# Optimization experiments

Hardware: AMD Instinct MI355X
Metric: run time of the kernel (lower is better)

## Reference

```python
import jax, jax.numpy as jnp
from jax import lax
import numpy as np

N, C, H, W = 8, 32, 64, 64
KS, NB = 7, 6            # kernel_size, num_bases
TB = (KS // 2) * NB      # total_bases = 18
BC = TB * NB             # bc_dim = 108
INTER = max(64, BC // 2) # 64
OUT = 64
PAD = KS // 2
EPS = 1e-5


def conv3x3(x, w, b):
    # x: (N,Cin,H,W), w: (Cout,Cin,3,3)
    y = lax.conv_general_dilated(x, w, (1, 1), [(1, 1), (1, 1)],
                                 dimension_numbers=('NCHW', 'OIHW', 'NCHW'))
    return y + b[None, :, None, None]


def batchnorm(x, g, b):
    # training-mode BN: batch stats over (N,H,W)
    mu = jnp.mean(x, axis=(0, 2, 3), keepdims=True)
    var = jnp.var(x, axis=(0, 2, 3), keepdims=True)
    return (x - mu) * lax.rsqrt(var + EPS) * g[None, :, None, None] + b[None, :, None, None]


def setup_inputs() -> dict:
    key = jax.random.key(0)
    ks = jax.random.split(key, 12)
    s = 0.05
    # random bases as in get_random_bases: (TB, KS*KS), zero-mean-ish rows
    f = jax.random.normal(ks[0], (TB, KS * KS), dtype=jnp.float32)
    bases = f - jnp.mean(f, axis=1, keepdims=True) / jnp.std(f, axis=1, keepdims=True)
    return {
        'x': jax.random.normal(ks[1], (N, C, H, W), dtype=jnp.float32),
        'conv1_w': jax.random.normal(ks[2], (INTER, C, 3, 3), dtype=jnp.float32) * s,
        'conv1_b': jax.random.normal(ks[3], (INTER,), dtype=jnp.float32) * s,
        'bn1_g': jnp.ones((INTER,), jnp.float32),
        'bn1_b': jnp.zeros((INTER,), jnp.float32),
        'conv2_w': jax.random.normal(ks[4], (BC, INTER, 3, 3), dtype=jnp.float32) * s,
        'conv2_b': jax.random.normal(ks[5], (BC,), dtype=jnp.float32) * s,
        'bn2_g': jnp.ones((BC,), jnp.float32),
        'bn2_b': jnp.zeros((BC,), jnp.float32),
        'bases': bases,
        'out_w': jax.random.normal(ks[6], (OUT, C * NB), dtype=jnp.float32) * s,
        'out_b': jax.random.normal(ks[7], (OUT,), dtype=jnp.float32) * s,
    }


def reference(x, conv1_w, conv1_b, bn1_g, bn1_b, conv2_w, conv2_b,
              bn2_g, bn2_b, bases, out_w, out_b):
    # bases_net: conv3x3 -> BN -> tanh -> conv3x3 -> BN -> tanh
    h = jnp.tanh(batchnorm(conv3x3(x, conv1_w, conv1_b), bn1_g, bn1_b))
    coef = jnp.tanh(batchnorm(conv3x3(h, conv2_w, conv2_b), bn2_g, bn2_b))
    # (N, BC, H, W) -> (N, NB, TB, H, W) -> (N, H, W, NB, TB)
    coef = coef.reshape(N, NB, TB, H, W).transpose(0, 3, 4, 1, 2)
    # atoms: (coef[...,None] * bases).sum(-2).transpose(-1,-2) => (N,H,W,KS^2,NB)
    atoms = jnp.einsum('nhwmt,tk->nhwkm', coef, bases)
    # unfold: channel-major (C, ks, ks) flattened, matching F.unfold
    patches = lax.conv_general_dilated_patches(
        x, (KS, KS), (1, 1), [(PAD, PAD), (PAD, PAD)],
        dimension_numbers=('NCHW', 'OIHW', 'NCHW'))  # (N, C*KS*KS, H, W)
    patches = patches.reshape(N, C, KS * KS, H, W)
    # per-pixel contraction over ks^2: (N,H,W,C,NB)
    bases_out = jnp.einsum('nckhw,nhwkm->nhwcm', patches, atoms)
    bases_out = bases_out.reshape(N, H, W, C * NB)
    out = jnp.einsum('nhwd,od->nohw', bases_out, out_w) + out_b[None, :, None, None]
    return out
```

## Files before the change

### kernel.cpp

```cpp
#include <hip/hip_runtime.h>
#include <hip/hip_bf16.h>

#define N_ 8
#define C_ 32
#define H_ 64
#define W_ 64
#define HW_ (H_*W_)
#define NHW_ (N_*HW_)
#define INTER_ 64
#define BC_ 108
#define KS_ 7
#define K2_ (KS_*KS_)
#define NB_ 6
#define TB_ 18
#define OUT_ 64
#define DDIM_ (C_*NB_)
#define P2CH_ 288

typedef __attribute__((ext_vector_type(8))) short short8;
typedef __attribute__((ext_vector_type(4))) float f32x4;

__device__ __forceinline__ unsigned short f2bf(float f) {
    union { float f; unsigned u; } v; v.f = f;
    unsigned r = v.u + 0x7fffu + ((v.u >> 16) & 1u);
    return (unsigned short)(r >> 16);
}
__device__ __forceinline__ float bf2f(unsigned short h) {
    return __uint_as_float((unsigned int)h << 16);
}

__device__ __forceinline__ short8 frag4(const unsigned int* p) {
    union { unsigned int u[4]; short8 s; } v;
    v.u[0] = p[0]; v.u[1] = p[1]; v.u[2] = p[2]; v.u[3] = p[3];
    return v.s;
}

__inline__ __device__ float wave_reduce_sum(float v) {
    #pragma unroll
    for (int off = 32; off > 0; off >>= 1) v += __shfl_down(v, off);
    return v;
}

__global__ __launch_bounds__(256) void k_front(const float* __restrict__ x,
                                               const float* __restrict__ bases,
                                               const float* __restrict__ w1,
                                               const float* __restrict__ w2,
                                               const float* __restrict__ ow,
                                               unsigned short* __restrict__ xb,
                                               unsigned short* __restrict__ wb1,
                                               unsigned short* __restrict__ wb2,
                                               unsigned short* __restrict__ wbp,
                                               unsigned int* __restrict__ P2) {
    __shared__ __align__(16) char smem[70 * 44 * 4];
    int bid = blockIdx.x, t = threadIdx.x;

    if (bid < 1024) {
        float (*sx)[44] = (float(*)[44])smem;
        int rq = bid & 3;
        int c  = (bid >> 2) & 31;
        int n  = bid >> 7;
        int lane = t & 63, wv = t >> 6;
        int r0 = rq << 4;

        const float* xc = x + (((size_t)n * C_ + c) << 12);
        #pragma unroll
        for (int j = 0; j < 6; j++) {
            int p = wv + 4 * j;
            if (p < 22) {
                int grow = r0 - 3 + p;
                bool rowok = (grow >= 0 && grow < H_);
                int wx = lane - 3;
                float v = 0.f;
                if (rowok && wx >= 0) v = xc[(grow << 6) + wx];
                sx[lane][p] = v;
                if (lane < 6) {
                    int wx2 = 61 + lane;
                    float v2 = 0.f;
                    if (rowok && wx2 < W_) v2 = xc[(grow << 6) + wx2];
                    sx[64 + lane][p] = v2;
                }
            }
        }
        __syncthreads();

        int rb = wv * 4;
        float a0[9][4], a1[9][4];
        #pragma unroll
        for (int tp = 0; tp < 9; tp++)
            #pragma unroll
            for (int rr = 0; rr < 4; rr++) { a0[tp][rr] = 0.f; a1[tp][rr] = 0.f; }

        #pragma unroll 1
        for (int kx = 0; kx < 7; kx++) {
            float rw[12];
            const float* sp = &sx[lane + kx][rb];
            #pragma unroll
            for (int qq = 0; qq < 3; qq++) {
                float4 r4 = *(const float4*)(sp + qq * 4);
                rw[qq * 4 + 0] = r4.x; rw[qq * 4 + 1] = r4.y;
                rw[qq * 4 + 2] = r4.z; rw[qq * 4 + 3] = r4.w;
            }
            #pragma unroll
            for (int tp = 0; tp < 9; tp++) {
                #pragma unroll
                for (int ky = 0; ky < 7; ky++) {
                    float w0 = bases[(2 * tp) * K2_ + ky * 7 + kx];
                    float w1v = bases[(2 * tp + 1) * K2_ + ky * 7 + kx];
                    #pragma unroll
                    for (int rr = 0; rr < 4; rr++) {
                        float xv = rw[rr + ky];
                        a0[tp][rr] += xv * w0;
                        a1[tp][rr] += xv * w1v;
                    }
                }
            }
        }

        #pragma unroll
        for (int tp = 0; tp < 9; tp++)
            #pragma unroll
            for (int rr = 0; rr < 4; rr++) {
                int gr = r0 + rb + rr;
                unsigned int pk = (unsigned int)f2bf(a0[tp][rr]) | ((unsigned int)f2bf(a1[tp][rr]) << 16);
                P2[(((size_t)n * P2CH_ + tp * 32 + c) << 12) + (gr << 6) + lane] = pk;
            }
    } else {
        int pbid = bid - 1024;
        if (pbid < 512) {
            unsigned short* sT = (unsigned short*)smem;
            int n = pbid >> 6, hw0 = (pbid << 6) & 4095;
            for (int i = t; i < 2048; i += 256) {
                int c = i >> 6, px = i & 63;
                float v = x[(((size_t)n * C_ + c) << 12) + hw0 + px];
                sT[px * 36 + c] = f2bf(v);
            }
            __syncthreads();
            unsigned int* xd = (unsigned int*)xb;
            for (int i = t; i < 1024; i += 256) {
                int px = i >> 4, cw = i & 15;
                unsigned int lo = sT[px * 36 + cw * 2], hi = sT[px * 36 + cw * 2 + 1];
                xd[(((size_t)n << 12) + hw0 + px) * 16 + cw] = lo | (hi << 16);
            }
        } else if (pbid < 584) {
            int i = (pbid - 512) * 256 + t;
            int ci = i & 31, co = (i >> 5) & 63, s = i >> 11;
            wb1[i] = f2bf(w1[((co << 5) + ci) * 9 + s]);
        } else if (pbid < 872) {
            int i = (pbid - 584) * 256 + t;
            int ci = i & 63, co = (i >> 6) & 127, s = i >> 13;
            unsigned short v = 0;
            if (co < BC_) v = f2bf(w2[((co << 6) + ci) * 9 + s]);
            wb2[i] = v;
        } else {
            int i = (pbid - 872) * 256 + t;
            if (i < OUT_ * DDIM_) {
                float v = ow[i];
                unsigned short hi = f2bf(v);
                wbp[i] = hi;
                wbp[OUT_ * DDIM_ + i] = f2bf(v - bf2f(hi));
            }
        }
    }
}

template<int CIN, int COG, int ROWS, int WPAD, int NCOQ>
__global__ __launch_bounds__(256) void k_conv3(const unsigned short* __restrict__ xb,
                                               const unsigned short* __restrict__ wb,
                                               const float* __restrict__ bias,
                                               float* __restrict__ y,
                                               int COUT_real) {
    constexpr int CPAD = CIN + 8;
    constexpr int NSLC = (ROWS + 2) * 66;
    constexpr int MT = COG / 16;
    constexpr int NTW = ROWS;
    constexpr int KSTEPS = CIN / 32;
    __shared__ unsigned short sx[NSLC * CPAD];
    __shared__ unsigned short sw[9 * COG * CPAD];

    int bid = blockIdx.x;
    int coq = bid % NCOQ;
    int rp = (bid / NCOQ) % (H_ / ROWS);
    int n = bid / (NCOQ * (H_ / ROWS));
    int h0 = rp * ROWS;
    int co0 = coq * COG;
    int t = threadIdx.x;
    int lane = t & 63, wv = t >> 6;
    int q = lane >> 4, n15 = lane & 15;

    {
        const unsigned int* xg = (const unsigned int*)xb + (size_t)n * HW_ * (CIN / 2);
        unsigned int* sxd = (unsigned int*)sx;
        constexpr int DW = CIN / 2;
        constexpr int DWPT = DW / 8;
        int part = t & 7;
        for (int sl = (t >> 3); sl < NSLC; sl += 32) {
            int r = sl / 66, col = sl % 66;
            int hh = h0 - 1 + r, ww = col - 1;
            unsigned int v[DWPT];
            #pragma unroll
            for (int i = 0; i < DWPT; i++) v[i] = 0;
            if (hh >= 0 && hh < H_ && ww >= 0 && ww < W_) {
                const unsigned int* gp = xg + (size_t)(hh * W_ + ww) * DW + part * DWPT;
                #pragma unroll
                for (int i = 0; i < DWPT; i++) v[i] = gp[i];
            }
            unsigned int* d = sxd + sl * (CPAD / 2) + part * DWPT;
            #pragma unroll
            for (int i = 0; i < DWPT; i++) d[i] = v[i];
        }
    }
    {
        const unsigned int* wg = (const unsigned int*)wb;
        unsigned int* swd = (unsigned int*)sw;
        constexpr int TOT = 9 * COG * (CIN / 2);
        for (int e = t; e < TOT; e += 256) {
            int s_co = e / (CIN / 2), cw = e % (CIN / 2);
            int s = s_co / COG, co = s_co % COG;
            swd[s_co * (CPAD / 2) + cw] = wg[((size_t)s * WPAD + co0 + co) * (CIN / 2) + cw];
        }
    }
    __syncthreads();

    f32x4 acc[NTW][MT];
    #pragma unroll
    for (int a = 0; a < NTW; a++)
        #pragma unroll
        for (int m = 0; m < MT; m++) acc[a][m] = (f32x4){0.f, 0.f, 0.f, 0.f};

    #pragma unroll
    for (int s = 0; s < 9; s++) {
        int dy = s / 3, dx = s % 3;
        #pragma unroll
        for (int kc = 0; kc < KSTEPS; kc++) {
            int ci0 = kc * 32;
            short8 bfr[NTW];
            #pragma unroll
            for (int ntl = 0; ntl < NTW; ntl++) {
                int nt = wv * NTW + ntl;
                int r_out = nt >> 2, col0 = (nt & 3) * 16;
                bfr[ntl] = *(const short8*)(sx + ((r_out + dy) * 66 + col0 + n15 + dx) * CPAD + ci0 + q * 8);
            }
            #pragma unroll
            for (int mt = 0; mt < MT; mt++) {
                short8 afr = *(const short8*)(sw + ((s * COG) + mt * 16 + n15) * CPAD + ci0 + q * 8);
                #pragma unroll
                for (int ntl = 0; ntl < NTW; ntl++)
                    acc[ntl][mt] = __builtin_amdgcn_mfma_f32_16x16x32_bf16(afr, bfr[ntl], acc[ntl][mt], 0, 0, 0);
            }
        }
    }

    #pragma unroll
    for (int ntl = 0; ntl < NTW; ntl++) {
        int nt = wv * NTW + ntl;
        int h = h0 + (nt >> 2), wcol = (nt & 3) * 16 + n15;
        #pragma unroll
        for (int mt = 0; mt < MT; mt++) {
            #pragma unroll
            for (int reg = 0; reg < 4; reg++) {
                int co = co0 + mt * 16 + q * 4 + reg;
                if (co < COUT_real)
                    y[(((size_t)n * COUT_real + co) << 12) + h * W_ + wcol] = acc[ntl][mt][reg] + bias[co];
            }
        }
    }
}

__global__ __launch_bounds__(256) void k_bnpart(const float* __restrict__ y,
                                                float2* __restrict__ part, int Cout) {
    int bid = blockIdx.x;
    int c = bid >> 3, n = bid & 7;
    int t = threadIdx.x;
    const float* p = y + (((size_t)n * Cout + c) << 12) + t * 16;
    float s = 0.f, s2 = 0.f;
    #pragma unroll
    for (int j = 0; j < 4; j++) {
        float4 v = *(const float4*)(p + j * 4);
        s += v.x + v.y + v.z + v.w;
        s2 += v.x * v.x + v.y * v.y + v.z * v.z + v.w * v.w;
    }
    s = wave_reduce_sum(s);
    s2 = wave_reduce_sum(s2);
    __shared__ float sm[8];
    int wid = t >> 6, lane = t & 63;
    if (lane == 0) { sm[wid] = s; sm[4 + wid] = s2; }
    __syncthreads();
    if (t == 0) {
        float2 r;
        r.x = sm[0] + sm[1] + sm[2] + sm[3];
        r.y = sm[4] + sm[5] + sm[6] + sm[7];
        part[c * 8 + n] = r;
    }
}

__global__ __launch_bounds__(256) void k_bntr(const float* __restrict__ y1,
                                              const float2* __restrict__ part,
                                              const float* __restrict__ g,
                                              const float* __restrict__ bb,
                                              unsigned short* __restrict__ y1b) {
    __shared__ unsigned short sT[64 * 68];
    __shared__ float scs[INTER_], shs[INTER_];
    int bid = blockIdx.x, t = threadIdx.x;
    int n = bid >> 6, hw0 = (bid << 6) & 4095;
    if (t < INTER_) {
        float s = 0.f, s2 = 0.f;
        #pragma unroll
        for (int j = 0; j < 8; j++) { float2 p = part[t * 8 + j]; s += p.x; s2 += p.y; }
        float mu = s / (float)NHW_, var = s2 / (float)NHW_ - mu * mu;
        float sc = g[t] * rsqrtf(var + 1e-5f);
        scs[t] = sc; shs[t] = bb[t] - mu * sc;
    }
    __syncthreads();
    for (int i = t; i < 4096; i += 256) {
        int c = i >> 6, px = i & 63;
        float v = y1[(((size_t)n * INTER_ + c) << 12) + hw0 + px];
        sT[px * 68 + c] = f2bf(tanhf(v * scs[c] + shs[c]));
    }
    __syncthreads();
    unsigned int* yd = (unsigned int*)y1b;
    for (int i = t; i < 2048; i += 256) {
        int px = i >> 5, cw = i & 31;
        unsigned int lo = sT[px * 68 + cw * 2], hi = sT[px * 68 + cw * 2 + 1];
        yd[(((size_t)n << 12) + hw0 + px) * 32 + cw] = lo | (hi << 16);
    }
}

#define YPAD_ 97
__global__ __launch_bounds__(256) void k_ytail(const float* __restrict__ y2,
                                               const float2* __restrict__ part,
                                               const float* __restrict__ g,
                                               const float* __restrict__ bb,
                                               const unsigned int* __restrict__ P2,
                                               const unsigned short* __restrict__ wbp,
                                               const float* __restrict__ out_b,
                                               float* __restrict__ out) {
    __shared__ float scs[BC_], shs[BC_];
    __shared__ float cfs[BC_][32];
    __shared__ unsigned int sYh[32 * YPAD_];
    __shared__ unsigned int sYl[32 * YPAD_];

    int bid = blockIdx.x;
    int n = bid >> 7, px0 = (bid & 127) << 5;
    int t = threadIdx.x;

    int px = t & 31, cg = t >> 5;
    unsigned int u[4][9];
    {
        const unsigned int* Pb = P2 + (((size_t)n * P2CH_) << 12) + px0 + px;
        #pragma unroll
        for (int cc = 0; cc < 4; cc++) {
            int c = cg * 4 + cc;
            #pragma unroll
            for (int tp = 0; tp < 9; tp++)
                u[cc][tp] = Pb[(size_t)(tp * 32 + c) << 12];
        }
    }

    if (t < BC_) {
        float s = 0.f, s2 = 0.f;
        #pragma unroll
        for (int j = 0; j < 8; j++) { float2 p = part[t * 8 + j]; s += p.x; s2 += p.y; }
        float mu = s / (float)NHW_, var = s2 / (float)NHW_ - mu * mu;
        float sc = g[t] * rsqrtf(var + 1e-5f);
        scs[t] = sc; shs[t] = bb[t] - mu * sc;
    }
    __syncthreads();

    for (int i = t; i < BC_ * 32; i += 256) {
        int ch = i >> 5, pxx = i & 31;
        float v = y2[(((size_t)n * BC_ + ch) << 12) + px0 + pxx];
        cfs[ch][pxx] = tanhf(v * scs[ch] + shs[ch]);
    }
    __syncthreads();

    {
        float pv[4][TB_];
        #pragma unroll
        for (int cc = 0; cc < 4; cc++)
            #pragma unroll
            for (int tp = 0; tp < 9; tp++) {
                pv[cc][2 * tp]     = __uint_as_float(u[cc][tp] << 16);
                pv[cc][2 * tp + 1] = __uint_as_float(u[cc][tp] & 0xffff0000u);
            }
        float ym[4][NB_];
        #pragma unroll
        for (int cc = 0; cc < 4; cc++)
            #pragma unroll
            for (int m = 0; m < NB_; m++) ym[cc][m] = 0.f;
        #pragma unroll
        for (int m = 0; m < NB_; m++)
            #pragma unroll
            for (int tt = 0; tt < TB_; tt++) {
                float cfv = cfs[m * TB_ + tt][px];
                #pragma unroll
                for (int cc = 0; cc < 4; cc++)
                    ym[cc][m] += cfv * pv[cc][tt];
            }
        #pragma unroll
        for (int cc = 0; cc < 4; cc++) {
            int c = cg * 4 + cc;
            #pragma unroll
            for (int j = 0; j < 3; j++) {
                unsigned short h0 = f2bf(ym[cc][2 * j]);
                unsigned short h1 = f2bf(ym[cc][2 * j + 1]);
                unsigned short l0 = f2bf(ym[cc][2 * j] - bf2f(h0));
                unsigned short l1 = f2bf(ym[cc][2 * j + 1] - bf2f(h1));
                sYh[px * YPAD_ + c * 3 + j] = (unsigned int)h0 | ((unsigned int)h1 << 16);
                sYl[px * YPAD_ + c * 3 + j] = (unsigned int)l0 | ((unsigned int)l1 << 16);
            }
        }
    }
    __syncthreads();

    int lane = t & 63, wv = t >> 6;
    int q = lane >> 4, n15 = lane & 15;
    f32x4 acc[2];
    acc[0] = (f32x4){0.f, 0.f, 0.f, 0.f};
    acc[1] = (f32x4){0.f, 0.f, 0.f, 0.f};
    #pragma unroll
    for (int ks = 0; ks < 6; ks++) {
        short8 ah = *(const short8*)(wbp + (wv * 16 + n15) * DDIM_ + ks * 32 + q * 8);
        short8 al = *(const short8*)(wbp + OUT_ * DDIM_ + (wv * 16 + n15) * DDIM_ + ks * 32 + q * 8);
        #pragma unroll
        for (int nt = 0; nt < 2; nt++) {
            short8 bh = frag4(sYh + (nt * 16 + n15) * YPAD_ + ks * 16 + q * 4);
            short8 bl = frag4(sYl + (nt * 16 + n15) * YPAD_ + ks * 16 + q * 4);
            acc[nt] = __builtin_amdgcn_mfma_f32_16x16x32_bf16(ah, bh, acc[nt], 0, 0, 0);
            acc[nt] = __builtin_amdgcn_mfma_f32_16x16x32_bf16(ah, bl, acc[nt], 0, 0, 0);
            acc[nt] = __builtin_amdgcn_mfma_f32_16x16x32_bf16(al, bh, acc[nt], 0, 0, 0);
        }
    }
    #pragma unroll
    for (int nt = 0; nt < 2; nt++)
        #pragma unroll
        for (int reg = 0; reg < 4; reg++) {
            int o = wv * 16 + q * 4 + reg;
            out[(((size_t)n * OUT_ + o) << 12) + px0 + nt * 16 + n15] = acc[nt][reg] + out_b[o];
        }
}

extern "C" void kernel_launch(void* const* d_in, const int* in_sizes, int n_in,
                              void* d_out, int out_size, void* d_ws, size_t ws_size,
                              hipStream_t stream) {
    const float* x       = (const float*)d_in[0];
    const float* conv1_w = (const float*)d_in[1];
    const float* conv1_b = (const float*)d_in[2];
    const float* bn1_g   = (const float*)d_in[3];
    const float* bn1_b   = (const float*)d_in[4];
    const float* conv2_w = (const float*)d_in[5];
    const float* conv2_b = (const float*)d_in[6];
    const float* bn2_g   = (const float*)d_in[7];
    const float* bn2_b   = (const float*)d_in[8];
    const float* bases   = (const float*)d_in[9];
    const float* out_w   = (const float*)d_in[10];
    const float* out_b   = (const float*)d_in[11];
    float* out = (float*)d_out;

    float* y1  = (float*)d_ws;
    float* y2  = y1 + (size_t)N_ * INTER_ * HW_;
    unsigned int* P2 = (unsigned int*)(y2 + (size_t)N_ * BC_ * HW_);
    unsigned short* xb  = (unsigned short*)(P2 + (size_t)N_ * P2CH_ * HW_);
    unsigned short* y1b = xb + (size_t)NHW_ * C_;
    unsigned short* wb1 = y1b + (size_t)NHW_ * INTER_;
    unsigned short* wb2 = wb1 + 9 * 64 * 32;
    unsigned short* wbp = wb2 + 9 * 128 * 64;
    float2* part1 = (float2*)(wbp + 2 * OUT_ * DDIM_);
    float2* part2 = part1 + INTER_ * 8;

    k_front<<<1944, 256, 0, stream>>>(x, bases, conv1_w, conv2_w, out_w,
                                      xb, wb1, wb2, wbp, P2);

    k_conv3<C_, 64, 1, 64, 1><<<N_ * 64, 256, 0, stream>>>(
        xb, wb1, conv1_b, y1, INTER_);
    k_bnpart<<<INTER_ * 8, 256, 0, stream>>>(y1, part1, INTER_);
    k_bntr<<<512, 256, 0, stream>>>(y1, part1, bn1_g, bn1_b, y1b);

    k_conv3<INTER_, 16, 2, 128, 7><<<N_ * 32 * 7, 256, 0, stream>>>(
        y1b, wb2, conv2_b, y2, BC_);
    k_bnpart<<<BC_ * 8, 256, 0, stream>>>(y2, part2, BC_);

    k_ytail<<<1024, 256, 0, stream>>>(y2, (const float2*)part2, bn2_g, bn2_b,
                                      P2, wbp, out_b, out);
}
```

Before: 196.2 us.

## Co-schedule patch-basis precompute with conv2 in one merged launch

The front kernel is split: the weight and input conversion stays in a small k_prep launch, while the per-channel patch×bases precompute (P2) moves into a new k_cpv kernel that interleaves it with conv2 blocks (7 conv blocks and 4 precompute blocks per group of 11). The aim is to overlap the ALU-heavy P2 work with the MFMA conv2 work and take it off the critical path ahead of conv1. In exchange, the shared-memory footprint is sized for the larger branch (about 58KB), which may lower occupancy for the conv blocks and makes the two workloads compete for the same compute units.

```diff
diff --git a/kernel.cpp b/kernel.cpp
--- a/kernel.cpp
+++ b/kernel.cpp
@@ -41,25 +41,249 @@
     return v;
 }
 
-__global__ __launch_bounds__(256) void k_front(const float* __restrict__ x,
-                                               const float* __restrict__ bases,
-                                               const float* __restrict__ w1,
-                                               const float* __restrict__ w2,
-                                               const float* __restrict__ ow,
-                                               unsigned short* __restrict__ xb,
-                                               unsigned short* __restrict__ wb1,
-                                               unsigned short* __restrict__ wb2,
-                                               unsigned short* __restrict__ wbp,
-                                               unsigned int* __restrict__ P2) {
-    __shared__ __align__(16) char smem[70 * 44 * 4];
+__global__ __launch_bounds__(256) void k_prep(const float* __restrict__ x,
+                                              const float* __restrict__ w1,
+                                              const float* __restrict__ w2,
+                                              const float* __restrict__ ow,
+                                              unsigned short* __restrict__ xb,
+                                              unsigned short* __restrict__ wb1,
+                                              unsigned short* __restrict__ wb2,
+                                              unsigned short* __restrict__ wbp) {
+    __shared__ unsigned short sT[64 * 36];
+    int pbid = blockIdx.x, t = threadIdx.x;
+    if (pbid < 512) {
+        int n = pbid >> 6, hw0 = (pbid << 6) & 4095;
+        for (int i = t; i < 2048; i += 256) {
+            int c = i >> 6, px = i & 63;
+            float v = x[(((size_t)n * C_ + c) << 12) + hw0 + px];
+            sT[px * 36 + c] = f2bf(v);
+        }
+        __syncthreads();
+        unsigned int* xd = (unsigned int*)xb;
+        for (int i = t; i < 1024; i += 256) {
+            int px = i >> 4, cw = i & 15;
+            unsigned int lo = sT[px * 36 + cw * 2], hi = sT[px * 36 + cw * 2 + 1];
+            xd[(((size_t)n << 12) + hw0 + px) * 16 + cw] = lo | (hi << 16);
+        }
+    } else if (pbid < 584) {
+        int i = (pbid - 512) * 256 + t;
+        int ci = i & 31, co = (i >> 5) & 63, s = i >> 11;
+        wb1[i] = f2bf(w1[((co << 5) + ci) * 9 + s]);
+    } else if (pbid < 872) {
+        int i = (pbid - 584) * 256 + t;
+        int ci = i & 63, co = (i >> 6) & 127, s = i >> 13;
+        unsigned short v = 0;
+        if (co < BC_) v = f2bf(w2[((co << 6) + ci) * 9 + s]);
+        wb2[i] = v;
+    } else {
+        int i = (pbid - 872) * 256 + t;
+        if (i < OUT_ * DDIM_) {
+            float v = ow[i];
+            unsigned short hi = f2bf(v);
+            wbp[i] = hi;
+            wbp[OUT_ * DDIM_ + i] = f2bf(v - bf2f(hi));
+        }
+    }
+}
+
+template<int CIN, int COG, int ROWS, int WPAD, int NCOQ>
+__global__ __launch_bounds__(256) void k_conv3(const unsigned short* __restrict__ xb,
+                                               const unsigned short* __restrict__ wb,
+                                               const float* __restrict__ bias,
+                                               float* __restrict__ y,
+                                               int COUT_real) {
+    constexpr int CPAD = CIN + 8;
+    constexpr int NSLC = (ROWS + 2) * 66;
+    constexpr int MT = COG / 16;
+    constexpr int NTW = ROWS;
+    constexpr int KSTEPS = CIN / 32;
+    __shared__ unsigned short sx[NSLC * CPAD];
+    __shared__ unsigned short sw[9 * COG * CPAD];
+
+    int bid = blockIdx.x;
+    int coq = bid % NCOQ;
+    int rp = (bid / NCOQ) % (H_ / ROWS);
+    int n = bid / (NCOQ * (H_ / ROWS));
+    int h0 = rp * ROWS;
+    int co0 = coq * COG;
+    int t = threadIdx.x;
+    int lane = t & 63, wv = t >> 6;
+    int q = lane >> 4, n15 = lane & 15;
+
+    {
+        const unsigned int* xg = (const unsigned int*)xb + (size_t)n * HW_ * (CIN / 2);
+        unsigned int* sxd = (unsigned int*)sx;
+        constexpr int DW = CIN / 2;
+        constexpr int DWPT = DW / 8;
+        int part = t & 7;
+        for (int sl = (t >> 3); sl < NSLC; sl += 32) {
+            int r = sl / 66, col = sl % 66;
+            int hh = h0 - 1 + r, ww = col - 1;
+            unsigned int v[DWPT];
+            #pragma unroll
+            for (int i = 0; i < DWPT; i++) v[i] = 0;
+            if (hh >= 0 && hh < H_ && ww >= 0 && ww < W_) {
+                const unsigned int* gp = xg + (size_t)(hh * W_ + ww) * DW + part * DWPT;
+                #pragma unroll
+                for (int i = 0; i < DWPT; i++) v[i] = gp[i];
+            }
+            unsigned int* d = sxd + sl * (CPAD / 2) + part * DWPT;
+            #pragma unroll
+            for (int i = 0; i < DWPT; i++) d[i] = v[i];
+        }
+    }
+    {
+        const unsigned int* wg = (const unsigned int*)wb;
+        unsigned int* swd = (unsigned int*)sw;
+        constexpr int TOT = 9 * COG * (CIN / 2);
+        for (int e = t; e < TOT; e += 256) {
+            int s_co = e / (CIN / 2), cw = e % (CIN / 2);
+            int s = s_co / COG, co = s_co % COG;
+            swd[s_co * (CPAD / 2) + cw] = wg[((size_t)s * WPAD + co0 + co) * (CIN / 2) + cw];
+        }
+    }
+    __syncthreads();
+
+    f32x4 acc[NTW][MT];
+    #pragma unroll
+    for (int a = 0; a < NTW; a++)
+        #pragma unroll
+        for (int m = 0; m < MT; m++) acc[a][m] = (f32x4){0.f, 0.f, 0.f, 0.f};
+
+    #pragma unroll
+    for (int s = 0; s < 9; s++) {
+        int dy = s / 3, dx = s % 3;
+        #pragma unroll
+        for (int kc = 0; kc < KSTEPS; kc++) {
+            int ci0 = kc * 32;
+            short8 bfr[NTW];
+            #pragma unroll
+            for (int ntl = 0; ntl < NTW; ntl++) {
+                int nt = wv * NTW + ntl;
+                int r_out = nt >> 2, col0 = (nt & 3) * 16;
+                bfr[ntl] = *(const short8*)(sx + ((r_out + dy) * 66 + col0 + n15 + dx) * CPAD + ci0 + q * 8);
+            }
+            #pragma unroll
+            for (int mt = 0; mt < MT; mt++) {
+                short8 afr = *(const short8*)(sw + ((s * COG) + mt * 16 + n15) * CPAD + ci0 + q * 8);
+                #pragma unroll
+                for (int ntl = 0; ntl < NTW; ntl++)
+                    acc[ntl][mt] = __builtin_amdgcn_mfma_f32_16x16x32_bf16(afr, bfr[ntl], acc[ntl][mt], 0, 0, 0);
+            }
+        }
+    }
+
+    #pragma unroll
+    for (int ntl = 0; ntl < NTW; ntl++) {
+        int nt = wv * NTW + ntl;
+        int h = h0 + (nt >> 2), wcol = (nt & 3) * 16 + n15;
+        #pragma unroll
+        for (int mt = 0; mt < MT; mt++) {
+            #pragma unroll
+            for (int reg = 0; reg < 4; reg++) {
+                int co = co0 + mt * 16 + q * 4 + reg;
+                if (co < COUT_real)
+                    y[(((size_t)n * COUT_real + co) << 12) + h * W_ + wcol] = acc[ntl][mt][reg] + bias[co];
+            }
+        }
+    }
+}
+
+__global__ __launch_bounds__(256) void k_cpv(const unsigned short* __restrict__ y1b,
+                                             const unsigned short* __restrict__ wb2,
+                                             const float* __restrict__ bias,
+                                             float* __restrict__ y2,
+                                             const float* __restrict__ x,
+                                             const float* __restrict__ bases,
+                                             unsigned int* __restrict__ P2) {
+    __shared__ __align__(16) char smem[58752];
     int bid = blockIdx.x, t = threadIdx.x;
-
-    if (bid < 1024) {
+    int grp = bid / 11, sub = bid % 11;
+    int lane = t & 63, wv = t >> 6;
+
+    if (sub < 7) {
+        constexpr int CPAD = 72, NSLC = 264;
+        unsigned short* sx = (unsigned short*)smem;
+        unsigned short* sw = sx + NSLC * CPAD;
+        int cid = grp * 7 + sub;
+        int coq = cid % 7;
+        int rp = (cid / 7) % 32;
+        int n = cid / (7 * 32);
+        int h0 = rp * 2;
+        int co0 = coq * 16;
+        int q = lane >> 4, n15 = lane & 15;
+
+        {
+            const unsigned int* xg = (const unsigned int*)y1b + (size_t)n * HW_ * 32;
+            unsigned int* sxd = (unsigned int*)sx;
+            int part = t & 7;
+            for (int sl = (t >> 3); sl < NSLC; sl += 32) {
+                int r = sl / 66, col = sl % 66;
+                int hh = h0 - 1 + r, ww = col - 1;
+                unsigned int v[4];
+                #pragma unroll
+                for (int i = 0; i < 4; i++) v[i] = 0;
+                if (hh >= 0 && hh < H_ && ww >= 0 && ww < W_) {
+                    const unsigned int* gp = xg + (size_t)(hh * W_ + ww) * 32 + part * 4;
+                    #pragma unroll
+                    for (int i = 0; i < 4; i++) v[i] = gp[i];
+                }
+                unsigned int* d = sxd + sl * 36 + part * 4;
+                #pragma unroll
+                for (int i = 0; i < 4; i++) d[i] = v[i];
+            }
+        }
+        {
+            const unsigned int* wg = (const unsigned int*)wb2;
+            unsigned int* swd = (unsigned int*)sw;
+            for (int e = t; e < 9 * 16 * 32; e += 256) {
+                int s_co = e / 32, cw = e % 32;
+                int s = s_co / 16, co = s_co % 16;
+                swd[s_co * 36 + cw] = wg[((size_t)s * 128 + co0 + co) * 32 + cw];
+            }
+        }
+        __syncthreads();
+
+        f32x4 acc[2];
+        acc[0] = (f32x4){0.f, 0.f, 0.f, 0.f};
+        acc[1] = (f32x4){0.f, 0.f, 0.f, 0.f};
+
+        #pragma unroll
+        for (int s = 0; s < 9; s++) {
+            int dy = s / 3, dx = s % 3;
+            #pragma unroll
+            for (int kc = 0; kc < 2; kc++) {
+                int ci0 = kc * 32;
+                short8 bfr[2];
+                #pragma unroll
+                for (int ntl = 0; ntl < 2; ntl++) {
+                    int nt = wv * 2 + ntl;
+                    int r_out = nt >> 2, col0 = (nt & 3) * 16;
+                    bfr[ntl] = *(const short8*)(sx + ((r_out + dy) * 66 + col0 + n15 + dx) * 72 + ci0 + q * 8);
+                }
+                short8 afr = *(const short8*)(sw + (s * 16 + n15) * 72 + ci0 + q * 8);
+                acc[0] = __builtin_amdgcn_mfma_f32_16x16x32_bf16(afr, bfr[0], acc[0], 0, 0, 0);
+                acc[1] = __builtin_amdgcn_mfma_f32_16x16x32_bf16(afr, bfr[1], acc[1], 0, 0, 0);
+            }
+        }
+
+        #pragma unroll
+        for (int ntl = 0; ntl < 2; ntl++) {
+            int nt = wv * 2 + ntl;
+            int h = h0 + (nt >> 2), wcol = (nt & 3) * 16 + n15;
+            #pragma unroll
+            for (int reg = 0; reg < 4; reg++) {
+                int co = co0 + q * 4 + reg;
+                if (co < BC_)
+                    y2[(((size_t)n * BC_ + co) << 12) + h * W_ + wcol] = acc[ntl][reg] + bias[co];
+            }
+        }
+    } else {
         float (*sx)[44] = (float(*)[44])smem;
-        int rq = bid & 3;
-        int c  = (bid >> 2) & 31;
-        int n  = bid >> 7;
-        int lane = t & 63, wv = t >> 6;
+        int pb = grp * 4 + (sub - 7);
+        int rq = pb & 3;
+        int c  = (pb >> 2) & 31;
+        int n  = pb >> 7;
         int r0 = rq << 4;
 
         const float* xc = x + (((size_t)n * C_ + c) << 12);
@@ -124,145 +348,6 @@
                 unsigned int pk = (unsigned int)f2bf(a0[tp][rr]) | ((unsigned int)f2bf(a1[tp][rr]) << 16);
                 P2[(((size_t)n * P2CH_ + tp * 32 + c) << 12) + (gr << 6) + lane] = pk;
             }
-    } else {
-        int pbid = bid - 1024;
-        if (pbid < 512) {
-            unsigned short* sT = (unsigned short*)smem;
-            int n = pbid >> 6, hw0 = (pbid << 6) & 4095;
-            for (int i = t; i < 2048; i += 256) {
-                int c = i >> 6, px = i & 63;
-                float v = x[(((size_t)n * C_ + c) << 12) + hw0 + px];
-                sT[px * 36 + c] = f2bf(v);
-            }
-            __syncthreads();
-            unsigned int* xd = (unsigned int*)xb;
-            for (int i = t; i < 1024; i += 256) {
-                int px = i >> 4, cw = i & 15;
-                unsigned int lo = sT[px * 36 + cw * 2], hi = sT[px * 36 + cw * 2 + 1];
-                xd[(((size_t)n << 12) + hw0 + px) * 16 + cw] = lo | (hi << 16);
-            }
-        } else if (pbid < 584) {
-            int i = (pbid - 512) * 256 + t;
-            int ci = i & 31, co = (i >> 5) & 63, s = i >> 11;
-            wb1[i] = f2bf(w1[((co << 5) + ci) * 9 + s]);
-        } else if (pbid < 872) {
-            int i = (pbid - 584) * 256 + t;
-            int ci = i & 63, co = (i >> 6) & 127, s = i >> 13;
-            unsigned short v = 0;
-            if (co < BC_) v = f2bf(w2[((co << 6) + ci) * 9 + s]);
-            wb2[i] = v;
-        } else {
-            int i = (pbid - 872) * 256 + t;
-            if (i < OUT_ * DDIM_) {
-                float v = ow[i];
-                unsigned short hi = f2bf(v);
-                wbp[i] = hi;
-                wbp[OUT_ * DDIM_ + i] = f2bf(v - bf2f(hi));
-            }
-        }
-    }
-}
-
-template<int CIN, int COG, int ROWS, int WPAD, int NCOQ>
-__global__ __launch_bounds__(256) void k_conv3(const unsigned short* __restrict__ xb,
-                                               const unsigned short* __restrict__ wb,
-                                               const float* __restrict__ bias,
-                                               float* __restrict__ y,
-                                               int COUT_real) {
-    constexpr int CPAD = CIN + 8;
-    constexpr int NSLC = (ROWS + 2) * 66;
-    constexpr int MT = COG / 16;
-    constexpr int NTW = ROWS;
-    constexpr int KSTEPS = CIN / 32;
-    __shared__ unsigned short sx[NSLC * CPAD];
-    __shared__ unsigned short sw[9 * COG * CPAD];
-
-    int bid = blockIdx.x;
-    int coq = bid % NCOQ;
-    int rp = (bid / NCOQ) % (H_ / ROWS);
-    int n = bid / (NCOQ * (H_ / ROWS));
-    int h0 = rp * ROWS;
-    int co0 = coq * COG;
-    int t = threadIdx.x;
-    int lane = t & 63, wv = t >> 6;
-    int q = lane >> 4, n15 = lane & 15;
-
-    {
-        const unsigned int* xg = (const unsigned int*)xb + (size_t)n * HW_ * (CIN / 2);
-        unsigned int* sxd = (unsigned int*)sx;
-        constexpr int DW = CIN / 2;
-        constexpr int DWPT = DW / 8;
-        int part = t & 7;
-        for (int sl = (t >> 3); sl < NSLC; sl += 32) {
-            int r = sl / 66, col = sl % 66;
-            int hh = h0 - 1 + r, ww = col - 1;
-            unsigned int v[DWPT];
-            #pragma unroll
-            for (int i = 0; i < DWPT; i++) v[i] = 0;
-            if (hh >= 0 && hh < H_ && ww >= 0 && ww < W_) {
-                const unsigned int* gp = xg + (size_t)(hh * W_ + ww) * DW + part * DWPT;
-                #pragma unroll
-                for (int i = 0; i < DWPT; i++) v[i] = gp[i];
-            }
-            unsigned int* d = sxd + sl * (CPAD / 2) + part * DWPT;
-            #pragma unroll
-            for (int i = 0; i < DWPT; i++) d[i] = v[i];
-        }
-    }
-    {
-        const unsigned int* wg = (const unsigned int*)wb;
-        unsigned int* swd = (unsigned int*)sw;
-        constexpr int TOT = 9 * COG * (CIN / 2);
-        for (int e = t; e < TOT; e += 256) {
-            int s_co = e / (CIN / 2), cw = e % (CIN / 2);
-            int s = s_co / COG, co = s_co % COG;
-            swd[s_co * (CPAD / 2) + cw] = wg[((size_t)s * WPAD + co0 + co) * (CIN / 2) + cw];
-        }
-    }
-    __syncthreads();
-
-    f32x4 acc[NTW][MT];
-    #pragma unroll
-    for (int a = 0; a < NTW; a++)
-        #pragma unroll
-        for (int m = 0; m < MT; m++) acc[a][m] = (f32x4){0.f, 0.f, 0.f, 0.f};
-
-    #pragma unroll
-    for (int s = 0; s < 9; s++) {
-        int dy = s / 3, dx = s % 3;
-        #pragma unroll
-        for (int kc = 0; kc < KSTEPS; kc++) {
-            int ci0 = kc * 32;
-            short8 bfr[NTW];
-            #pragma unroll
-            for (int ntl = 0; ntl < NTW; ntl++) {
-                int nt = wv * NTW + ntl;
-                int r_out = nt >> 2, col0 = (nt & 3) * 16;
-                bfr[ntl] = *(const short8*)(sx + ((r_out + dy) * 66 + col0 + n15 + dx) * CPAD + ci0 + q * 8);
-            }
-            #pragma unroll
-            for (int mt = 0; mt < MT; mt++) {
-                short8 afr = *(const short8*)(sw + ((s * COG) + mt * 16 + n15) * CPAD + ci0 + q * 8);
-                #pragma unroll
-                for (int ntl = 0; ntl < NTW; ntl++)
-                    acc[ntl][mt] = __builtin_amdgcn_mfma_f32_16x16x32_bf16(afr, bfr[ntl], acc[ntl][mt], 0, 0, 0);
-            }
-        }
-    }
-
-    #pragma unroll
-    for (int ntl = 0; ntl < NTW; ntl++) {
-        int nt = wv * NTW + ntl;
-        int h = h0 + (nt >> 2), wcol = (nt & 3) * 16 + n15;
-        #pragma unroll
-        for (int mt = 0; mt < MT; mt++) {
-            #pragma unroll
-            for (int reg = 0; reg < 4; reg++) {
-                int co = co0 + mt * 16 + q * 4 + reg;
-                if (co < COUT_real)
-                    y[(((size_t)n * COUT_real + co) << 12) + h * W_ + wcol] = acc[ntl][mt][reg] + bias[co];
-            }
-        }
     }
 }
 
@@ -467,16 +552,14 @@
     float2* part1 = (float2*)(wbp + 2 * OUT_ * DDIM_);
     float2* part2 = part1 + INTER_ * 8;
 
-    k_front<<<1944, 256, 0, stream>>>(x, bases, conv1_w, conv2_w, out_w,
-                                      xb, wb1, wb2, wbp, P2);
+    k_prep<<<920, 256, 0, stream>>>(x, conv1_w, conv2_w, out_w, xb, wb1, wb2, wbp);
 
     k_conv3<C_, 64, 1, 64, 1><<<N_ * 64, 256, 0, stream>>>(
         xb, wb1, conv1_b, y1, INTER_);
     k_bnpart<<<INTER_ * 8, 256, 0, stream>>>(y1, part1, INTER_);
     k_bntr<<<512, 256, 0, stream>>>(y1, part1, bn1_g, bn1_b, y1b);
 
-    k_conv3<INTER_, 16, 2, 128, 7><<<N_ * 32 * 7, 256, 0, stream>>>(
-        y1b, wb2, conv2_b, y2, BC_);
+    k_cpv<<<2816, 256, 0, stream>>>(y1b, wb2, conv2_b, y2, x, bases, P2);
     k_bnpart<<<BC_ * 8, 256, 0, stream>>>(y2, part2, BC_);
 
     k_ytail<<<1024, 256, 0, stream>>>(y2, (const float2*)part2, bn2_g, bn2_b,
```

After: 207.4 us. 5.7% more time.
